# Performance work log

Measured on AMD Instinct MI355X. Metric: run time of the kernel, lower is better.

## Reference

```python
import jax, jax.numpy as jnp
import numpy as np

B, SEQ, DIM = 1, 2048, 4096
N_HEADS, N_KV, HEAD_DIM = 32, 8, 128
N_REP = N_HEADS // N_KV
MAX_CTX = 4096


def setup_inputs() -> dict:
    key = jax.random.key(0)
    ks = jax.random.split(key, 6)
    x = jax.random.normal(ks[0], (B, SEQ, DIM), jnp.float32)
    # RoPE table: (1, SEQ, 1, HEAD_DIM//2, 2) with [cos, sin] in last dim
    inv_freq = 1.0 / (10000.0 ** (jnp.arange(0, HEAD_DIM, 2, dtype=jnp.float32) / HEAD_DIM))
    t = jnp.arange(SEQ, dtype=jnp.float32)
    ang = t[:, None] * inv_freq[None, :]
    freqs_cis = jnp.stack([jnp.cos(ang), jnp.sin(ang)], axis=-1).reshape(1, SEQ, 1, HEAD_DIM // 2, 2)
    cache_kv = jnp.zeros((2, 1, MAX_CTX, N_KV, HEAD_DIM), jnp.float32)
    s = 0.02
    wq = jax.random.normal(ks[1], (DIM, N_HEADS * HEAD_DIM), jnp.float32) * s
    wk = jax.random.normal(ks[2], (DIM, N_KV * HEAD_DIM), jnp.float32) * s
    wv = jax.random.normal(ks[3], (DIM, N_KV * HEAD_DIM), jnp.float32) * s
    wo = jax.random.normal(ks[4], (N_HEADS * HEAD_DIM, DIM), jnp.float32) * s
    return {"x": x, "cache_kv": cache_kv, "freqs_cis": freqs_cis,
            "wq": wq, "wk": wk, "wv": wv, "wo": wo, "start_pos": 0}


def _rope(t, freqs_cis):
    # t: (b, s, h, head_dim); freqs_cis: (1, s, 1, head_dim//2, 2)
    tr = t.reshape(*t.shape[:-1], -1, 2)
    a, b = tr[..., 0], tr[..., 1]
    c, d = freqs_cis[..., 0], freqs_cis[..., 1]
    return jnp.stack([a * c - b * d, a * d + b * c], axis=-1).reshape(t.shape)


def reference(x, cache_kv, freqs_cis, wq, wk, wv, wo, start_pos):
    b, s, _ = x.shape
    xq = (x @ wq).reshape(b, s, N_HEADS, HEAD_DIM)
    xk = (x @ wk).reshape(b, s, N_KV, HEAD_DIM)
    xv = (x @ wv).reshape(b, s, N_KV, HEAD_DIM)
    xq = _rope(xq, freqs_cis)
    xk = _rope(xk, freqs_cis)
    # KV-cache scatter write (start_pos is a static Python int)
    cache = cache_kv.at[:, :, start_pos:start_pos + s].set(jnp.stack([xk, xv]))
    L = start_pos + s
    keys = cache[0, :, :L]    # (b, L, kv, hd)
    values = cache[1, :, :L]
    # GQA without materializing repeats: group q heads by kv head
    q = xq.transpose(0, 2, 1, 3).reshape(b, N_KV, N_REP, s, HEAD_DIM)
    k = keys.transpose(0, 2, 1, 3)     # (b, kv, L, hd)
    v = values.transpose(0, 2, 1, 3)
    scores = jnp.einsum('bkrqd,bkld->bkrql', q, k) * (HEAD_DIM ** -0.5)
    if s > 1:
        mask = jnp.triu(jnp.full((s, L), -jnp.inf, jnp.float32), k=start_pos + 1)
        scores = scores + mask
    p = jax.nn.softmax(scores, axis=-1)
    out = jnp.einsum('bkrql,bkld->bkrqd', p, v)          # (b, kv, rep, s, hd)
    out = out.reshape(b, N_HEADS, s, HEAD_DIM).transpose(0, 2, 1, 3).reshape(b, s, N_HEADS * HEAD_DIM)
    return out @ wo
```

## Files before the change

### kernel.cpp

```cpp
#include <hip/hip_runtime.h>
#include <hip/hip_bf16.h>
#include <stdint.h>

#define SEQ   2048
#define DIM   4096
#define NH    32
#define NKV   8
#define HD    128
#define NREP  4
#define QKVN  6144
#define KOFF  4096
#define VOFF  5120

typedef __bf16 bf16;
typedef __attribute__((ext_vector_type(8))) __bf16 bf16x8;
typedef __attribute__((ext_vector_type(4))) __bf16 bf16x4;
typedef __attribute__((ext_vector_type(4))) float  f32x4;
typedef __attribute__((address_space(1))) void as1_void;
typedef __attribute__((address_space(3))) void as3_void;

__device__ __forceinline__ void async_copy16(void* lds, const void* g) {
  __builtin_amdgcn_global_load_lds((as1_void*)(void*)g, (as3_void*)lds, 16, 0, 0);
}

__device__ __forceinline__ uint32_t pack2bf(float a, float b) {
  union { bf16 h; uint16_t u; } ca, cb;
  ca.h = (bf16)a; cb.h = (bf16)b;
  return (uint32_t)ca.u | ((uint32_t)cb.u << 16);
}

__device__ __forceinline__ void block_barrier() {
  asm volatile("" ::: "memory");
  __builtin_amdgcn_s_barrier();
  asm volatile("" ::: "memory");
}

__global__ __launch_bounds__(256) void cast_x_kernel(const float* __restrict__ src,
                                                     bf16* __restrict__ dst) {
  size_t i = ((size_t)blockIdx.x * 256 + threadIdx.x) * 4;
  const float4 v = *(const float4*)(src + i);
  bf16x4 o;
  o[0] = (bf16)v.x; o[1] = (bf16)v.y; o[2] = (bf16)v.z; o[3] = (bf16)v.w;
  *(bf16x4*)(dst + i) = o;
}

__global__ __launch_bounds__(256) void transpose_cast_kernel(const float* __restrict__ src,
                                                             bf16* __restrict__ dst,
                                                             int R, int C) {
  __shared__ float tile[64][65];
  const int c0 = blockIdx.x * 64, r0 = blockIdx.y * 64;
  const int tx = threadIdx.x & 15, ty = threadIdx.x >> 4;
#pragma unroll
  for (int p = 0; p < 4; ++p) {
    float4 v = *(const float4*)&src[(size_t)(r0 + ty + p*16) * C + c0 + tx*4];
    tile[ty + p*16][tx*4+0] = v.x;
    tile[ty + p*16][tx*4+1] = v.y;
    tile[ty + p*16][tx*4+2] = v.z;
    tile[ty + p*16][tx*4+3] = v.w;
  }
  __syncthreads();
  const int k = threadIdx.x & 15;
  const int g = threadIdx.x >> 4;
#pragma unroll
  for (int p = 0; p < 4; ++p) {
    int X = g + 16*p;
    bf16x4 o;
    o[0] = (bf16)tile[4*k+0][X];
    o[1] = (bf16)tile[4*k+1][X];
    o[2] = (bf16)tile[4*k+2][X];
    o[3] = (bf16)tile[4*k+3][X];
    *(bf16x4*)&dst[(size_t)(c0 + X) * R + r0 + 4*k] = o;
  }
}

template<int OUT_F32, int ROPE, int BN>
__global__ __launch_bounds__(512, 2) void gemm256_kernel(const bf16* __restrict__ A,
                                                         const bf16* __restrict__ Bt,
                                                         void* __restrict__ Cout,
                                                         int M, int N, int K,
                                                         const float* __restrict__ fr) {
  constexpr int BNF = BN / 64;
  constexpr int BCH = BN / 64;
  constexpr int BBYTES = BN * 128;
  __shared__ __align__(16) char lds[65536 + 2 * BBYTES];

  const int tid  = threadIdx.x;
  const int w    = tid >> 6, lane = tid & 63;
  const int lane16 = lane & 15, quad = lane >> 4;
  const int wm = w >> 2, wn = w & 3;

  const int nwg = gridDim.x * gridDim.y;
  int bid = blockIdx.y * gridDim.x + blockIdx.x;
  bid = (bid & 7) * (nwg >> 3) + (bid >> 3);
  const int bx = bid % gridDim.x, by = bid / gridDim.x;
  const int bm = by * 256, bn = bx * BN;

  const int NT = K >> 6;

  auto stageA = [&](int buf, int t, int ks) {
#pragma unroll
    for (int i = 0; i < 2; ++i) {
      int c = tid + (i << 9);
      int q = c >> 8, row = c & 255;
      async_copy16(lds + buf*32768 + ks*16384 + c*16,
                   A + (size_t)(bm + row) * K + t*64 + ks*32 + q*8);
    }
  };
  auto stageB = [&](int buf, int t) {
#pragma unroll
    for (int i = 0; i < BCH; ++i) {
      int c = tid + (i << 9);
      int ks = c / (BN*4), r = c - ks*(BN*4);
      int q = r / BN, col = r - q*BN;
      async_copy16(lds + 65536 + buf*BBYTES + c*16,
                   Bt + (size_t)(bn + col) * K + t*64 + ks*32 + q*8);
    }
  };

  f32x4 acc[8][BNF] = {};

#define LD_A(DST, BUF, KS, QM)                                                        \
  do {                                                                                \
    _Pragma("unroll")                                                                 \
    for (int ii = 0; ii < 4; ++ii)                                                    \
      (DST)[ii] = *(const bf16x8*)(lds + (BUF)*32768 + (KS)*16384 +                   \
          (quad*256 + wm*128 + (QM)*64 + ii*16 + lane16) * 16);                       \
  } while (0)
#define LD_B(DST, BUF, KS)                                                            \
  do {                                                                                \
    _Pragma("unroll")                                                                 \
    for (int jj = 0; jj < BNF; ++jj)                                                  \
      (DST)[jj] = *(const bf16x8*)(lds + 65536 + (BUF)*BBYTES +                       \
          (((KS)*4 + quad)*BN + wn*(BN/4) + jj*16 + lane16) * 16);                    \
  } while (0)
#define MMA_PHASE(AF, BF, QM)                                                         \
  do {                                                                                \
    asm volatile("s_waitcnt lgkmcnt(0)" ::: "memory");                                \
    __builtin_amdgcn_sched_barrier(0);                                                \
    __builtin_amdgcn_s_setprio(1);                                                    \
    _Pragma("unroll")                                                                 \
    for (int jj = 0; jj < BNF; ++jj)                                                  \
      _Pragma("unroll")                                                               \
      for (int ii = 0; ii < 4; ++ii)                                                  \
        acc[(QM)*4 + ii][jj] = __builtin_amdgcn_mfma_f32_16x16x32_bf16(               \
            (AF)[ii], (BF)[jj], acc[(QM)*4 + ii][jj], 0, 0, 0);                       \
    __builtin_amdgcn_s_setprio(0);                                                    \
  } while (0)
#define VM_WAIT_STEADY()                                                              \
  do {                                                                                \
    if constexpr (BN == 192) asm volatile("s_waitcnt vmcnt(7)" ::: "memory");         \
    else                     asm volatile("s_waitcnt vmcnt(6)" ::: "memory");         \
  } while (0)

  stageA(0, 0, 0); stageB(0, 0); stageA(0, 0, 1);
  stageA(1, 1, 0); stageB(1, 1);
  VM_WAIT_STEADY();
  block_barrier();

  for (int t = 0; t < NT; ++t) {
    const int cb = t & 1, nb = cb ^ 1;
    bf16x8 af[4], bf0[BNF], bf1[BNF];

    LD_A(af, cb, 0, 0);
    LD_B(bf0, cb, 0);
    if (t + 1 < NT) stageA(nb, t + 1, 1);
    block_barrier();
    MMA_PHASE(af, bf0, 0);
    block_barrier();

    LD_A(af, cb, 0, 1);
    block_barrier();
    MMA_PHASE(af, bf0, 1);
    if (t + 1 < NT) VM_WAIT_STEADY();
    else            asm volatile("s_waitcnt vmcnt(0)" ::: "memory");
    block_barrier();

    LD_A(af, cb, 1, 0);
    LD_B(bf1, cb, 1);
    if (t + 2 < NT) stageA(cb, t + 2, 0);
    block_barrier();
    MMA_PHASE(af, bf1, 0);
    block_barrier();

    LD_A(af, cb, 1, 1);
    if (t + 2 < NT) stageB(cb, t + 2);
    block_barrier();
    MMA_PHASE(af, bf1, 1);
    if (t + 2 < NT)      VM_WAIT_STEADY();
    else if (t + 1 < NT) asm volatile("s_waitcnt vmcnt(2)" ::: "memory");
    else                 asm volatile("s_waitcnt vmcnt(0)" ::: "memory");
    block_barrier();
  }

#pragma unroll
  for (int i = 0; i < 8; ++i)
#pragma unroll
    for (int j = 0; j < BNF; ++j) {
      const int colb = bn + wn*(BN/4) + j*16;
      const bool do_rope = ROPE && colb < 5120;
      const int p2 = (colb + lane16) & 126;
#pragma unroll
      for (int r = 0; r < 4; ++r) {
        size_t row = (size_t)bm + wm*128 + i*16 + quad*4 + r;
        size_t col = (size_t)colb + lane16;
        float v = acc[i][j][r];
        if (ROPE) {
          float vp = __shfl_xor(v, 1);
          if (do_rope) {
            float2 cd = *(const float2*)&fr[row*128 + p2];
            v = (lane16 & 1) ? (vp*cd.y + v*cd.x) : (v*cd.x - vp*cd.y);
          }
        }
        if (OUT_F32) ((float*)Cout)[row * N + col] = v;
        else         ((bf16*)Cout)[row * N + col] = (bf16)v;
      }
    }
#undef LD_A
#undef LD_B
#undef MMA_PHASE
#undef VM_WAIT_STEADY
}

__global__ __launch_bounds__(256) void transpose_v_kernel(const bf16* __restrict__ qkv,
                                                          bf16* __restrict__ vt) {
  __shared__ bf16 tile[32][33];
  int tt = blockIdx.x * 32;
  int dd = blockIdx.y * 32;
  int kv = blockIdx.z;
  int tx = threadIdx.x & 31, ty = threadIdx.x >> 5;
  const bf16* src = qkv + VOFF + kv * HD;
#pragma unroll
  for (int j = 0; j < 4; ++j)
    tile[ty + j*8][tx] = src[(size_t)(tt + ty + j*8) * QKVN + dd + tx];
  __syncthreads();
  bf16* dst = vt + ((size_t)kv * HD + dd) * SEQ + tt;
#pragma unroll
  for (int j = 0; j < 4; ++j)
    dst[(size_t)(ty + j*8) * SEQ + tx] = tile[tx][ty + j*8];
}

__global__ __launch_bounds__(256, 3) void flash_attn_kernel(const bf16* __restrict__ qkv,
                                                            const bf16* __restrict__ vt,
                                                            bf16* __restrict__ out) {
  __shared__ __align__(16) bf16 Ks[4*96*32];
  __shared__ __align__(16) bf16 Vts[3*128*32];
  const int b  = blockIdx.x;
  const int qt = 31 - (b >> 5);
  const int h  = b & 31;
  const int kvh = h >> 2;
  const int tid = threadIdx.x;
  const int w = tid >> 6, lane = tid & 63;
  const int lane16 = lane & 15, quad = lane >> 4;
  const float scale = 0.08838834764831845f;
  const int qglob = qt*64 + w*16 + lane16;

  const bf16* qrow = qkv + (size_t)qglob * QKVN + h * HD + quad*8;
  bf16x8 qreg[4];
#pragma unroll
  for (int kk = 0; kk < 4; ++kk)
    qreg[kk] = *(const bf16x8*)(qrow + kk*32);

  f32x4 acc_o[8] = {};
  float m_s = -3e38f, l_s = 0.f;

  const bf16* kbase0 = qkv + KOFF + kvh * HD;
  const bf16* vbase0 = vt + (size_t)kvh * HD * SEQ;

  const int L = (qt*64 + 159) / 96;
  for (int jj = 0; jj < L; ++jj) {
    const int kv0 = jj * 96;
    __syncthreads();
#pragma unroll
    for (int i = 0; i < 6; ++i) {
      int c = tid + i * 256;
      {
        int kk = c / 384, rem = c - kk*384;
        async_copy16(&Ks[c*8], kbase0 + (size_t)(kv0 + (rem >> 2)) * QKVN + kk*32 + (rem & 3) * 8);
      }
      {
        int kk2 = c >> 9, cp = c & 511;
        async_copy16(&Vts[c*8], vbase0 + (size_t)(cp >> 2) * SEQ + kv0 + kk2*32 + (cp & 3) * 8);
      }
    }
    __syncthreads();

    f32x4 accT[6] = {};
#pragma unroll
    for (int kk = 0; kk < 4; ++kk)
#pragma unroll
      for (int jn = 0; jn < 6; ++jn) {
        bf16x8 kf = *(const bf16x8*)&Ks[(kk*96 + jn*16 + lane16)*32 + quad*8];
        accT[jn] = __builtin_amdgcn_mfma_f32_16x16x32_bf16(kf, qreg[kk], accT[jn], 0, 0, 0);
      }

    float s[6][4];
#pragma unroll
    for (int jn = 0; jn < 6; ++jn)
#pragma unroll
      for (int r = 0; r < 4; ++r) {
        float v = accT[jn][r] * scale;
        if ((kv0 + jn*16 + quad*4 + r) > qglob) v = -3e38f;
        s[jn][r] = v;
      }

    float mt = s[0][0];
#pragma unroll
    for (int jn = 0; jn < 6; ++jn)
#pragma unroll
      for (int r = 0; r < 4; ++r) mt = fmaxf(mt, s[jn][r]);
    mt = fmaxf(mt, __shfl_xor(mt, 16));
    mt = fmaxf(mt, __shfl_xor(mt, 32));
    float mnew = fmaxf(m_s, mt);
    float alpha = __expf(m_s - mnew);
    m_s = mnew;
    float rs = 0.f;
#pragma unroll
    for (int jn = 0; jn < 6; ++jn)
#pragma unroll
      for (int r = 0; r < 4; ++r) {
        float p = __expf(s[jn][r] - mnew);
        s[jn][r] = p;
        rs += p;
      }
    rs += __shfl_xor(rs, 16);
    rs += __shfl_xor(rs, 32);
    l_s = l_s * alpha + rs;

    float alpha_row[4];
#pragma unroll
    for (int r = 0; r < 4; ++r)
      alpha_row[r] = __shfl(alpha, quad*4 + r);
#pragma unroll
    for (int jd = 0; jd < 8; ++jd)
#pragma unroll
      for (int r = 0; r < 4; ++r) acc_o[jd][r] *= alpha_row[r];

    uint32_t pk[6][2];
#pragma unroll
    for (int jn = 0; jn < 6; ++jn) {
      pk[jn][0] = pack2bf(s[jn][0], s[jn][1]);
      pk[jn][1] = pack2bf(s[jn][2], s[jn][3]);
    }

    const int src0 = (quad & 1) * 32 + lane16;
    const int src1 = src0 + 16;
    const bool hi = quad >= 2;
#pragma unroll
    for (int kk2 = 0; kk2 < 3; ++kk2) {
      uint32_t v0l = __shfl(pk[2*kk2][0],   src0), v0h = __shfl(pk[2*kk2][1],   src0);
      uint32_t v1l = __shfl(pk[2*kk2][0],   src1), v1h = __shfl(pk[2*kk2][1],   src1);
      uint32_t w0l = __shfl(pk[2*kk2+1][0], src0), w0h = __shfl(pk[2*kk2+1][1], src0);
      uint32_t w1l = __shfl(pk[2*kk2+1][0], src1), w1h = __shfl(pk[2*kk2+1][1], src1);
      union { uint32_t u[4]; bf16x8 v; } af;
      af.u[0] = hi ? w0l : v0l;
      af.u[1] = hi ? w0h : v0h;
      af.u[2] = hi ? w1l : v1l;
      af.u[3] = hi ? w1h : v1h;
#pragma unroll
      for (int jd = 0; jd < 8; ++jd) {
        bf16x8 vf = *(const bf16x8*)&Vts[(kk2*128 + jd*16 + lane16)*32 + quad*8];
        acc_o[jd] = __builtin_amdgcn_mfma_f32_16x16x32_bf16(af.v, vf, acc_o[jd], 0, 0, 0);
      }
    }
  }

  const float inv_l = 1.f / l_s;
  float linv[4];
#pragma unroll
  for (int r = 0; r < 4; ++r)
    linv[r] = __shfl(inv_l, quad*4 + r);

  bf16* obase = out + (size_t)(qt*64 + w*16) * DIM + h * HD;
#pragma unroll
  for (int jd = 0; jd < 8; ++jd)
#pragma unroll
    for (int r = 0; r < 4; ++r)
      obase[(size_t)(quad*4 + r) * DIM + jd*16 + lane16] = (bf16)(acc_o[jd][r] * linv[r]);
}

extern "C" void kernel_launch(void* const* d_in, const int* in_sizes, int n_in,
                              void* d_out, int out_size, void* d_ws, size_t ws_size,
                              hipStream_t stream) {
  const float* x  = (const float*)d_in[0];
  const float* fr = (const float*)d_in[2];
  const float* wq = (const float*)d_in[3];
  const float* wk = (const float*)d_in[4];
  const float* wv = (const float*)d_in[5];
  const float* wo = (const float*)d_in[6];
  float* out = (float*)d_out;

  char* ws = (char*)d_ws;
  bf16* xb     = (bf16*)(ws);
  bf16* wqkv_t = (bf16*)(ws + 16777216);
  bf16* wo_t   = (bf16*)(ws + 67108864);
  bf16* qkv    = (bf16*)(ws + 100663296);
  bf16* vt     = (bf16*)(ws + 125829120);
  bf16* attn   = (bf16*)(ws + 130023424);
  (void)ws_size; (void)in_sizes; (void)n_in; (void)out_size;

  cast_x_kernel<<<8192, 256, 0, stream>>>(x, xb);
  transpose_cast_kernel<<<dim3(64,64), 256, 0, stream>>>(wq, wqkv_t, DIM, DIM);
  transpose_cast_kernel<<<dim3(16,64), 256, 0, stream>>>(wk, wqkv_t + (size_t)4096*4096, DIM, 1024);
  transpose_cast_kernel<<<dim3(16,64), 256, 0, stream>>>(wv, wqkv_t + (size_t)5120*4096, DIM, 1024);
  transpose_cast_kernel<<<dim3(64,64), 256, 0, stream>>>(wo, wo_t, DIM, DIM);

  gemm256_kernel<0,1,192><<<dim3(32,8), 512, 0, stream>>>(xb, wqkv_t, qkv, SEQ, QKVN, DIM, fr);
  transpose_v_kernel<<<dim3(64,4,8), 256, 0, stream>>>(qkv, vt);
  flash_attn_kernel<<<1024, 256, 0, stream>>>(qkv, vt, attn);
  gemm256_kernel<1,0,128><<<dim3(32,8), 512, 0, stream>>>(attn, wo_t, out, SEQ, DIM, DIM, nullptr);
}
```

Baseline: 621.1 us.

## Restructure GEMM main loop with XOR-swizzled LDS and triple-buffered B

Changes the GEMM LDS layout to row-major 128-byte rows with an XOR swizzle on 16-byte slots, so fragment reads avoid bank conflicts. B tiles become triple-buffered while A stays double-buffered. The per-iteration schedule drops from eight barriers to two, letting LDS reads and MFMAs interleave without explicit lgkmcnt waits. This adds LDS use, which may affect the two-blocks-per-CU occupancy, and changes the vmcnt accounting, which could be fragile.

```diff
diff --git a/kernel.cpp b/kernel.cpp
--- a/kernel.cpp
+++ b/kernel.cpp
@@ -81,8 +81,9 @@
                                                          const float* __restrict__ fr) {
   constexpr int BNF = BN / 64;
   constexpr int BCH = BN / 64;
-  constexpr int BBYTES = BN * 128;
-  __shared__ __align__(16) char lds[65536 + 2 * BBYTES];
+  constexpr int BBUF = BN * 128;
+  __shared__ __align__(16) char ldsA[2 * 32768];
+  __shared__ __align__(16) char ldsB[3 * BBUF];
 
   const int tid  = threadIdx.x;
   const int w    = tid >> 6, lane = tid & 63;
@@ -97,23 +98,22 @@
 
   const int NT = K >> 6;
 
-  auto stageA = [&](int buf, int t, int ks) {
-#pragma unroll
-    for (int i = 0; i < 2; ++i) {
+  auto stageA = [&](int buf, int t) {
+#pragma unroll
+    for (int i = 0; i < 4; ++i) {
       int c = tid + (i << 9);
-      int q = c >> 8, row = c & 255;
-      async_copy16(lds + buf*32768 + ks*16384 + c*16,
-                   A + (size_t)(bm + row) * K + t*64 + ks*32 + q*8);
+      int row = c >> 3, sl = c & 7;
+      async_copy16(ldsA + buf*32768 + c*16,
+                   A + (size_t)(bm + row) * K + t*64 + ((sl ^ (row & 7)) << 3));
     }
   };
   auto stageB = [&](int buf, int t) {
 #pragma unroll
     for (int i = 0; i < BCH; ++i) {
       int c = tid + (i << 9);
-      int ks = c / (BN*4), r = c - ks*(BN*4);
-      int q = r / BN, col = r - q*BN;
-      async_copy16(lds + 65536 + buf*BBYTES + c*16,
-                   Bt + (size_t)(bn + col) * K + t*64 + ks*32 + q*8);
+      int col = c >> 3, sl = c & 7;
+      async_copy16(ldsB + buf*BBUF + c*16,
+                   Bt + (size_t)(bn + col) * K + t*64 + ((sl ^ (col & 7)) << 3));
     }
   };
 
@@ -122,21 +122,23 @@
 #define LD_A(DST, BUF, KS, QM)                                                        \
   do {                                                                                \
     _Pragma("unroll")                                                                 \
-    for (int ii = 0; ii < 4; ++ii)                                                    \
-      (DST)[ii] = *(const bf16x8*)(lds + (BUF)*32768 + (KS)*16384 +                   \
-          (quad*256 + wm*128 + (QM)*64 + ii*16 + lane16) * 16);                       \
+    for (int ii = 0; ii < 4; ++ii) {                                                  \
+      int row_ = wm*128 + (QM)*64 + ii*16 + lane16;                                   \
+      int S_ = ((KS)*4 + quad) ^ (lane16 & 7);                                        \
+      (DST)[ii] = *(const bf16x8*)(ldsA + (BUF)*32768 + row_*128 + S_*16);            \
+    }                                                                                 \
   } while (0)
 #define LD_B(DST, BUF, KS)                                                            \
   do {                                                                                \
     _Pragma("unroll")                                                                 \
-    for (int jj = 0; jj < BNF; ++jj)                                                  \
-      (DST)[jj] = *(const bf16x8*)(lds + 65536 + (BUF)*BBYTES +                       \
-          (((KS)*4 + quad)*BN + wn*(BN/4) + jj*16 + lane16) * 16);                    \
+    for (int jj = 0; jj < BNF; ++jj) {                                                \
+      int col_ = wn*(BN/4) + jj*16 + lane16;                                          \
+      int S_ = ((KS)*4 + quad) ^ (lane16 & 7);                                        \
+      (DST)[jj] = *(const bf16x8*)(ldsB + (BUF)*BBUF + col_*128 + S_*16);             \
+    }                                                                                 \
   } while (0)
-#define MMA_PHASE(AF, BF, QM)                                                         \
+#define MMA_BATCH(AF, BF, QM)                                                         \
   do {                                                                                \
-    asm volatile("s_waitcnt lgkmcnt(0)" ::: "memory");                                \
-    __builtin_amdgcn_sched_barrier(0);                                                \
     __builtin_amdgcn_s_setprio(1);                                                    \
     _Pragma("unroll")                                                                 \
     for (int jj = 0; jj < BNF; ++jj)                                                  \
@@ -146,49 +148,35 @@
             (AF)[ii], (BF)[jj], acc[(QM)*4 + ii][jj], 0, 0, 0);                       \
     __builtin_amdgcn_s_setprio(0);                                                    \
   } while (0)
-#define VM_WAIT_STEADY()                                                              \
-  do {                                                                                \
-    if constexpr (BN == 192) asm volatile("s_waitcnt vmcnt(7)" ::: "memory");         \
-    else                     asm volatile("s_waitcnt vmcnt(6)" ::: "memory");         \
-  } while (0)
-
-  stageA(0, 0, 0); stageB(0, 0); stageA(0, 0, 1);
-  stageA(1, 1, 0); stageB(1, 1);
-  VM_WAIT_STEADY();
+
+  stageB(0, 0); stageA(0, 0); stageB(1, 1); stageA(1, 1);
+  asm volatile("s_waitcnt vmcnt(%0)" :: "i"(4 + BCH) : "memory");
   block_barrier();
 
   for (int t = 0; t < NT; ++t) {
-    const int cb = t & 1, nb = cb ^ 1;
-    bf16x8 af[4], bf0[BNF], bf1[BNF];
-
-    LD_A(af, cb, 0, 0);
-    LD_B(bf0, cb, 0);
-    if (t + 1 < NT) stageA(nb, t + 1, 1);
+    const int ca = t & 1;
+    const int cbb = t % 3;
+    if (t + 2 < NT) stageB((t + 2) % 3, t + 2);
+
+    bf16x8 af[4], b0[BNF], b1[BNF];
+    LD_B(b0, cbb, 0);
+    LD_A(af, ca, 0, 0);
+    MMA_BATCH(af, b0, 0);
+    LD_A(af, ca, 0, 1);
+    MMA_BATCH(af, b0, 1);
+    LD_B(b1, cbb, 1);
+    LD_A(af, ca, 1, 0);
+    MMA_BATCH(af, b1, 0);
+    LD_A(af, ca, 1, 1);
+    MMA_BATCH(af, b1, 1);
+
     block_barrier();
-    MMA_PHASE(af, bf0, 0);
-    block_barrier();
-
-    LD_A(af, cb, 0, 1);
-    block_barrier();
-    MMA_PHASE(af, bf0, 1);
-    if (t + 1 < NT) VM_WAIT_STEADY();
-    else            asm volatile("s_waitcnt vmcnt(0)" ::: "memory");
-    block_barrier();
-
-    LD_A(af, cb, 1, 0);
-    LD_B(bf1, cb, 1);
-    if (t + 2 < NT) stageA(cb, t + 2, 0);
-    block_barrier();
-    MMA_PHASE(af, bf1, 0);
-    block_barrier();
-
-    LD_A(af, cb, 1, 1);
-    if (t + 2 < NT) stageB(cb, t + 2);
-    block_barrier();
-    MMA_PHASE(af, bf1, 1);
-    if (t + 2 < NT)      VM_WAIT_STEADY();
-    else if (t + 1 < NT) asm volatile("s_waitcnt vmcnt(2)" ::: "memory");
-    else                 asm volatile("s_waitcnt vmcnt(0)" ::: "memory");
+    if (t + 2 < NT) {
+      stageA(ca, t + 2);
+      asm volatile("s_waitcnt vmcnt(%0)" :: "i"(4 + BCH) : "memory");
+    } else {
+      asm volatile("s_waitcnt vmcnt(0)" ::: "memory");
+    }
     block_barrier();
   }
 
@@ -217,8 +205,7 @@
     }
 #undef LD_A
 #undef LD_B
-#undef MMA_PHASE
-#undef VM_WAIT_STEADY
+#undef MMA_BATCH
 }
 
 __global__ __launch_bounds__(256) void transpose_v_kernel(const bf16* __restrict__ qkv,
```

New measurement: 581.5 us. 1.07x faster.
